# Optimization experiments

Hardware: AMD Instinct MI355X
Metric: run time of the kernel (lower is better)

Reference implementation:

```python
import jax, jax.numpy as jnp
import numpy as np

B, S, E = 4, 2048, 1024
H, D = 16, 64  # num_heads, attention_head_dim


def setup_inputs() -> dict:
    key = jax.random.key(0)
    ks = jax.random.split(key, 9)
    scale_e = 1.0 / np.sqrt(E)
    scale_hd = 1.0 / np.sqrt(H * D)
    x = jax.random.normal(ks[0], (B, S, E), dtype=jnp.float32)
    # per-head projection weights, stacked: [H, E, D]
    Wq = jax.random.uniform(ks[1], (H, E, D), minval=-scale_e, maxval=scale_e, dtype=jnp.float32)
    Wk = jax.random.uniform(ks[2], (H, E, D), minval=-scale_e, maxval=scale_e, dtype=jnp.float32)
    Wv = jax.random.uniform(ks[3], (H, E, D), minval=-scale_e, maxval=scale_e, dtype=jnp.float32)
    bq = jax.random.uniform(ks[4], (H, D), minval=-scale_e, maxval=scale_e, dtype=jnp.float32)
    bk = jax.random.uniform(ks[5], (H, D), minval=-scale_e, maxval=scale_e, dtype=jnp.float32)
    bv = jax.random.uniform(ks[6], (H, D), minval=-scale_e, maxval=scale_e, dtype=jnp.float32)
    Wo = jax.random.uniform(ks[7], (H * D, E), minval=-scale_hd, maxval=scale_hd, dtype=jnp.float32)
    bo = jax.random.uniform(ks[8], (E,), minval=-scale_hd, maxval=scale_hd, dtype=jnp.float32)
    return {"x": x, "Wq": Wq, "Wk": Wk, "Wv": Wv, "bq": bq, "bk": bk, "bv": bv, "Wo": Wo, "bo": bo}


def reference(x, Wq, Wk, Wv, bq, bk, bv, Wo, bo):
    # Per-head QKV projections, vectorized over heads: [B,H,S,D]
    Q = jnp.einsum('bse,hed->bhsd', x, Wq) + bq[None, :, None, :]
    K = jnp.einsum('bse,hed->bhsd', x, Wk) + bk[None, :, None, :]
    V = jnp.einsum('bse,hed->bhsd', x, Wv) + bv[None, :, None, :]
    scale = 1.0 / jnp.sqrt(jnp.asarray(D, dtype=Q.dtype))
    scores = jnp.einsum('bhsd,bhtd->bhst', Q, K) * scale  # [B,H,S,S]
    attn = jax.nn.softmax(scores, axis=-1)
    Z = jnp.einsum('bhst,bhtd->bhsd', attn, V)            # [B,H,S,D]
    # concat heads on feature dim -> [B,S,H*D], then output projection
    Zc = jnp.transpose(Z, (0, 2, 1, 3)).reshape(B, S, H * D)
    return Zc @ Wo + bo
```

## Files before the change

kernel.cpp:

```cpp
#include <hip/hip_runtime.h>


typedef __attribute__((ext_vector_type(4)))  float   f32x4;
typedef __attribute__((ext_vector_type(16))) float   f32x16;
typedef __attribute__((ext_vector_type(8)))  __bf16  bf16x8;
typedef __attribute__((ext_vector_type(4)))  __bf16  bf16x4;
typedef __attribute__((ext_vector_type(4)))  unsigned int u32x4;
typedef unsigned int u32;

#if __has_builtin(__builtin_amdgcn_exp2f)
#define EXP2F(x) __builtin_amdgcn_exp2f(x)
#else
#define EXP2F(x) exp2f(x)
#endif

__device__ __forceinline__ f32x4 fzero4() {
    f32x4 z = {0.f, 0.f, 0.f, 0.f};
    return z;
}
__device__ __forceinline__ f32x16 fzero16() {
    f32x16 z;
#pragma unroll
    for (int i = 0; i < 16; i++) z[i] = 0.f;
    return z;
}

__device__ __forceinline__ u32 cvtpk_bf16(float lo, float hi_) {
    u32 r;
    asm("v_cvt_pk_bf16_f32 %0, %1, %2" : "=v"(r) : "v"(lo), "v"(hi_));
    return r;
}

__device__ __forceinline__ void gload_lds16(const void* g, void* l) {
    __builtin_amdgcn_global_load_lds(
        (const __attribute__((address_space(1))) u32*)g,
        (__attribute__((address_space(3))) u32*)l, 16, 0, 0);
}

__global__ __launch_bounds__(256) void cvt_f32_bf16_4(
    const float* __restrict__ s, __bf16* __restrict__ d, long n) {
    long i = ((long)blockIdx.x * 256 + threadIdx.x) * 4;
    if (i >= n) return;
    float4 v = *(const float4*)(s + i);
    bf16x4 o = { (__bf16)v.x, (__bf16)v.y, (__bf16)v.z, (__bf16)v.w };
    *(bf16x4*)(d + i) = o;
}

__global__ __launch_bounds__(256) void pack_w_t(
    const float* __restrict__ src, __bf16* __restrict__ dst, int R, int C) {
    __shared__ float t[32][33];
    const int z = blockIdx.z;
    src += (size_t)z * R * C;
    dst += (size_t)z * R * C;
    const int r0 = blockIdx.x * 32, c0 = blockIdx.y * 32;
    const int x = threadIdx.x, y = threadIdx.y;
#pragma unroll
    for (int i = 0; i < 4; i++)
        t[y + i * 8][x] = src[(size_t)(r0 + y + i * 8) * C + c0 + x];
    __syncthreads();
#pragma unroll
    for (int i = 0; i < 4; i++)
        dst[(size_t)(c0 + y + i * 8) * R + r0 + x] = (__bf16)t[x][y + i * 8];
}

__global__ __launch_bounds__(256) void pack_bias(
    const float* __restrict__ bq, const float* __restrict__ bk,
    const float* __restrict__ bv, float* __restrict__ bqkv) {
    int n = blockIdx.x * 256 + threadIdx.x;
    if (n >= 3072) return;
    int t = n >> 10, r = n & 1023;
    const float* s = (t == 0) ? bq : (t == 1) ? bk : bv;
    bqkv[n] = s[r];
}

template <bool F32OUT>
__global__ __launch_bounds__(256) void gemm_bt(
    const __bf16* __restrict__ A, const __bf16* __restrict__ Bt,
    const float* __restrict__ bias, void* __restrict__ Cout,
    int M, int N, int K, int ldc) {
    __shared__ __bf16 As[128 * 32];
    __shared__ __bf16 Bs[128 * 32];
    const int tid  = threadIdx.x;
    const int lane = tid & 63, wid = tid >> 6;
    const int wr = wid >> 1, wc = wid & 1;
    const int l15 = lane & 15, l4 = lane >> 4;
    const int bn = blockIdx.x, bm = blockIdx.y;
    const long arow = (long)bm * 128 + (tid >> 2);
    const long brow = (long)bn * 128 + (tid >> 2);
    const int  kcol = (tid & 3) * 8;

    f32x4 acc[4][4];
#pragma unroll
    for (int i = 0; i < 4; i++)
#pragma unroll
        for (int j = 0; j < 4; j++) acc[i][j] = fzero4();

    for (int k0 = 0; k0 < K; k0 += 32) {
        gload_lds16(A + arow * K + k0 + kcol,        (char*)As + wid * 1024);
        gload_lds16(A + (arow + 64) * K + k0 + kcol, (char*)As + 4096 + wid * 1024);
        gload_lds16(Bt + brow * K + k0 + kcol,        (char*)Bs + wid * 1024);
        gload_lds16(Bt + (brow + 64) * K + k0 + kcol, (char*)Bs + 4096 + wid * 1024);
        __syncthreads();
        bf16x8 a[4], b[4];
#pragma unroll
        for (int mi = 0; mi < 4; mi++)
            a[mi] = *(const bf16x8*)&As[(wr * 64 + mi * 16 + l15) * 32 + l4 * 8];
#pragma unroll
        for (int ni = 0; ni < 4; ni++)
            b[ni] = *(const bf16x8*)&Bs[(wc * 64 + ni * 16 + l15) * 32 + l4 * 8];
#pragma unroll
        for (int mi = 0; mi < 4; mi++)
#pragma unroll
            for (int ni = 0; ni < 4; ni++)
                acc[mi][ni] = __builtin_amdgcn_mfma_f32_16x16x32_bf16(
                    a[mi], b[ni], acc[mi][ni], 0, 0, 0);
        __syncthreads();
    }

#pragma unroll
    for (int mi = 0; mi < 4; mi++)
#pragma unroll
        for (int ni = 0; ni < 4; ni++) {
            const int row = bm * 128 + wr * 64 + mi * 16 + l4 * 4;
            const int col = bn * 128 + wc * 64 + ni * 16 + l15;
            const float bv = bias ? bias[col] : 0.f;
#pragma unroll
            for (int r = 0; r < 4; r++) {
                float v = acc[mi][ni][r] + bv;
                if (F32OUT)
                    ((float*)Cout)[(long)(row + r) * ldc + col] = v;
                else
                    ((__bf16*)Cout)[(long)(row + r) * ldc + col] = (__bf16)v;
            }
        }
}

__global__ __launch_bounds__(256) void repack_vt(
    const __bf16* __restrict__ QKV, __bf16* __restrict__ VT) {
    __shared__ __bf16 t[32][33];
    const int s0 = blockIdx.x * 32, d0 = blockIdx.y * 32, bh = blockIdx.z;
    const int b = bh >> 4, h = bh & 15;
    const int x = threadIdx.x, y = threadIdx.y;
    const __bf16* src = QKV + (size_t)(b * 2048) * 3072 + 2048 + h * 64;
#pragma unroll
    for (int i = 0; i < 4; i++)
        t[y + i * 8][x] = src[(size_t)(s0 + y + i * 8) * 3072 + d0 + x];
    __syncthreads();
    __bf16* dst = VT + (size_t)bh * 64 * 2048;
#pragma unroll
    for (int i = 0; i < 4; i++)
        dst[(size_t)(d0 + y + i * 8) * 2048 + s0 + x] = t[x][y + i * 8];
}

__global__ __launch_bounds__(256, 4) void attn_fwd(
    const __bf16* __restrict__ QKV, const __bf16* __restrict__ VT,
    __bf16* __restrict__ Z) {
    const int S = 2048, LDQ = 3072;
    const int dd = blockIdx.x;
    const int blk = (dd & 7) * 128 + (dd >> 3);
    const int qt = blk & 15, bh = blk >> 4, b = bh >> 4, h = bh & 15;
    const int tid = threadIdx.x, wid = tid >> 6, lane = tid & 63;
    const int l31 = lane & 31, hi = lane >> 5;

    __shared__ __bf16 smem[16384];

    const __bf16* Qb = QKV + (size_t)b * S * LDQ + h * 64;
    const __bf16* Kb = Qb + 1024;
    const __bf16* Vb = VT + (size_t)bh * 64 * S;
    const int qrow = qt * 128 + wid * 32;

    bf16x8 qf[4];
#pragma unroll
    for (int kk = 0; kk < 4; kk++)
        qf[kk] = *(const bf16x8*)(Qb + (size_t)(qrow + l31) * LDQ + kk * 16 + hi * 8);

    const int f0 = wid * 2, f1 = wid * 2 + 1;
    const int kr0 = (f0 >> 2) * 32 + l31, kc0 = (f0 & 3) * 16 + hi * 8;
    const int kr1 = (f1 >> 2) * 32 + l31, kc1 = (f1 & 3) * 16 + hi * 8;
    const int vr0 = kr0, vs0 = kc0;
    const int vr1 = kr1, vs1 = kc1;
    const int ldst = lane * 16;

    f32x16 o0 = fzero16(), o1 = fzero16();
    float m_r = -1e30f, l_r = 0.f;
    const float csc = 0.18033688011f;

    gload_lds16(Kb + (size_t)kr0 * LDQ + kc0, (char*)smem + f0 * 1024 + ldst);
    gload_lds16(Kb + (size_t)kr1 * LDQ + kc1, (char*)smem + f1 * 1024 + ldst);
    gload_lds16(Vb + (size_t)vr0 * S + vs0,   (char*)smem + 16384 + f0 * 1024 + ldst);
    gload_lds16(Vb + (size_t)vr1 * S + vs1,   (char*)smem + 16384 + f1 * 1024 + ldst);
    asm volatile("s_waitcnt vmcnt(0)" ::: "memory");
    __syncthreads();

    int cur = 0;
    for (int t0 = 0; t0 < S; t0 += 64, cur ^= 1) {
        if (t0 + 64 < S) {
            char* kl = (char*)smem + (cur ^ 1) * 8192;
            char* vl = (char*)smem + 16384 + (cur ^ 1) * 8192;
            gload_lds16(Kb + (size_t)(t0 + 64 + kr0) * LDQ + kc0, kl + f0 * 1024 + ldst);
            gload_lds16(Kb + (size_t)(t0 + 64 + kr1) * LDQ + kc1, kl + f1 * 1024 + ldst);
            gload_lds16(Vb + (size_t)vr0 * S + t0 + 64 + vs0,     vl + f0 * 1024 + ldst);
            gload_lds16(Vb + (size_t)vr1 * S + t0 + 64 + vs1,     vl + f1 * 1024 + ldst);
        }
        const char* kbase = (const char*)smem + cur * 8192;
        const char* vbase = (const char*)smem + 16384 + cur * 8192;

        bf16x8 kf[8];
#pragma unroll
        for (int f = 0; f < 8; f++)
            kf[f] = *(const bf16x8*)(kbase + f * 1024 + ldst);
        f32x16 s0 = fzero16(), s1 = fzero16();
        __builtin_amdgcn_s_setprio(1);
#pragma unroll
        for (int kk = 0; kk < 4; kk++) {
            s0 = __builtin_amdgcn_mfma_f32_32x32x16_bf16(kf[kk],     qf[kk], s0, 0, 0, 0);
            s1 = __builtin_amdgcn_mfma_f32_32x32x16_bf16(kf[4 + kk], qf[kk], s1, 0, 0, 0);
        }
        __builtin_amdgcn_s_setprio(0);

        float mm[16];
#pragma unroll
        for (int i = 0; i < 16; i++) mm[i] = fmaxf(s0[i], s1[i]);
#pragma unroll
        for (int st = 8; st >= 1; st >>= 1)
#pragma unroll
            for (int i = 0; i < st; i++) mm[i] = fmaxf(mm[i], mm[i + st]);
        const float pm = fmaxf(mm[0], __shfl_xor(mm[0], 32));
        const float mnew = fmaxf(m_r, pm);
        const float alpha = EXP2F((m_r - mnew) * csc);
        m_r = mnew;
        l_r *= alpha;
#pragma unroll
        for (int i = 0; i < 16; i++) { o0[i] *= alpha; o1[i] *= alpha; }
        const float mc = m_r * csc;
        float ss[16];
#pragma unroll
        for (int i = 0; i < 16; i++) {
            float p0 = EXP2F(s0[i] * csc - mc); s0[i] = p0;
            float p1 = EXP2F(s1[i] * csc - mc); s1[i] = p1;
            ss[i] = p0 + p1;
        }
#pragma unroll
        for (int st = 8; st >= 1; st >>= 1)
#pragma unroll
            for (int i = 0; i < st; i++) ss[i] += ss[i + st];
        l_r += ss[0] + __shfl_xor(ss[0], 32);

#pragma unroll
        for (int kkt = 0; kkt < 4; kkt++) {
            const int r0 = (kkt & 1) * 8;
            u32 w0, w1, w2, w3;
            if (kkt < 2) {
                w0 = cvtpk_bf16(s0[r0],     s0[r0 + 1]);
                w1 = cvtpk_bf16(s0[r0 + 2], s0[r0 + 3]);
                w2 = cvtpk_bf16(s0[r0 + 4], s0[r0 + 5]);
                w3 = cvtpk_bf16(s0[r0 + 6], s0[r0 + 7]);
            } else {
                w0 = cvtpk_bf16(s1[r0],     s1[r0 + 1]);
                w1 = cvtpk_bf16(s1[r0 + 2], s1[r0 + 3]);
                w2 = cvtpk_bf16(s1[r0 + 4], s1[r0 + 5]);
                w3 = cvtpk_bf16(s1[r0 + 6], s1[r0 + 7]);
            }
            asm("v_permlane32_swap_b32 %0, %1" : "+v"(w0), "+v"(w2));
            asm("v_permlane32_swap_b32 %0, %1" : "+v"(w1), "+v"(w3));
            u32x4 pw = {w0, w1, w2, w3};
            bf16x8 pf = __builtin_bit_cast(bf16x8, pw);
            bf16x8 vf0 = *(const bf16x8*)(vbase + kkt * 1024 + ldst);
            bf16x8 vf1 = *(const bf16x8*)(vbase + (4 + kkt) * 1024 + ldst);
            __builtin_amdgcn_s_setprio(1);
            o0 = __builtin_amdgcn_mfma_f32_32x32x16_bf16(vf0, pf, o0, 0, 0, 0);
            o1 = __builtin_amdgcn_mfma_f32_32x32x16_bf16(vf1, pf, o1, 0, 0, 0);
            __builtin_amdgcn_s_setprio(0);
        }

        asm volatile("s_waitcnt vmcnt(0)" ::: "memory");
        __syncthreads();
    }

    const float inv = 1.0f / l_r;
    __bf16 (*Tl)[72] = (__bf16 (*)[72])smem;
    const int trow = wid * 32 + l31;
#pragma unroll
    for (int g = 0; g < 4; g++) {
        bf16x4 t4a, t4b;
#pragma unroll
        for (int j = 0; j < 4; j++) {
            t4a[j] = (__bf16)(o0[4 * g + j] * inv);
            t4b[j] = (__bf16)(o1[4 * g + j] * inv);
        }
        *(bf16x4*)&Tl[trow][g * 8 + hi * 4]      = t4a;
        *(bf16x4*)&Tl[trow][32 + g * 8 + hi * 4] = t4b;
    }
    asm volatile("s_waitcnt lgkmcnt(0)" ::: "memory");
    __builtin_amdgcn_sched_barrier(0);

    const int rr = wid * 32 + (lane >> 1);
    const int ch = (lane & 1) * 32;
#pragma unroll
    for (int i = 0; i < 4; i++) {
        bf16x8 z = *(const bf16x8*)&Tl[rr][ch + i * 8];
        *(bf16x8*)&Z[((size_t)b * S + qt * 128 + rr) * 1024 + h * 64 + ch + i * 8] = z;
    }
}

extern "C" void kernel_launch(void* const* d_in, const int* in_sizes, int n_in,
                              void* d_out, int out_size, void* d_ws, size_t ws_size,
                              hipStream_t stream) {
    const float* x  = (const float*)d_in[0];
    const float* Wq = (const float*)d_in[1];
    const float* Wk = (const float*)d_in[2];
    const float* Wv = (const float*)d_in[3];
    const float* bq = (const float*)d_in[4];
    const float* bk = (const float*)d_in[5];
    const float* bv = (const float*)d_in[6];
    const float* Wo = (const float*)d_in[7];
    const float* bo = (const float*)d_in[8];
    float* out = (float*)d_out;

    char* p = (char*)d_ws;
    __bf16* xb   = (__bf16*)p; p += 8192L * 1024 * 2;
    __bf16* Wqkv = (__bf16*)p; p += 3072L * 1024 * 2;
    float*  bqkv = (float*)p;  p += 3072L * 4;
    __bf16* QKV  = (__bf16*)p; p += 8192L * 3072 * 2;
    __bf16* VTb  = (__bf16*)p; p += 64L * 64 * 2048 * 2;
    __bf16* Zb   = (__bf16*)p; p += 8192L * 1024 * 2;
    __bf16* Wot  = (__bf16*)p; p += 1024L * 1024 * 2;

    cvt_f32_bf16_4<<<8192, 256, 0, stream>>>(x, xb, 8192L * 1024);
    pack_w_t<<<dim3(32, 2, 16), dim3(32, 8), 0, stream>>>(Wq, Wqkv,                1024, 64);
    pack_w_t<<<dim3(32, 2, 16), dim3(32, 8), 0, stream>>>(Wk, Wqkv + 1024L * 1024, 1024, 64);
    pack_w_t<<<dim3(32, 2, 16), dim3(32, 8), 0, stream>>>(Wv, Wqkv + 2048L * 1024, 1024, 64);
    pack_w_t<<<dim3(32, 32, 1), dim3(32, 8), 0, stream>>>(Wo, Wot, 1024, 1024);
    pack_bias<<<12, 256, 0, stream>>>(bq, bk, bv, bqkv);

    gemm_bt<false><<<dim3(24, 64), 256, 0, stream>>>(xb, Wqkv, bqkv, QKV,
                                                     8192, 3072, 1024, 3072);
    repack_vt<<<dim3(64, 2, 64), dim3(32, 8), 0, stream>>>(QKV, VTb);
    attn_fwd<<<1024, 256, 0, stream>>>(QKV, VTb, Zb);
    gemm_bt<true><<<dim3(8, 64), 256, 0, stream>>>(Zb, Wot, bo, out,
                                                   8192, 1024, 1024, 1024);
}
```

Measured before the change: 234.3 us.

## Fuse V transpose into QKV GEMM epilogue and skip unneeded softmax rescales

A dedicated QKV GEMM now writes the V slice straight into the transposed VT layout from its epilogue, so the separate repack_vt kernel launch and its extra read/write of V go away. The attention loop only rescales the running max and accumulators when some lane's new max exceeds the old one by more than a threshold (lazy rescaling). This avoids the exp and 32 multiplies per tile in the common case, but relies on the stale max keeping exp2 bounded. The priority raise is also hoisted to cover the whole PV MFMA loop instead of toggling per iteration.

```diff
diff --git a/kernel.cpp b/kernel.cpp
--- a/kernel.cpp
+++ b/kernel.cpp
@@ -135,21 +135,80 @@
         }
 }
 
-__global__ __launch_bounds__(256) void repack_vt(
-    const __bf16* __restrict__ QKV, __bf16* __restrict__ VT) {
-    __shared__ __bf16 t[32][33];
-    const int s0 = blockIdx.x * 32, d0 = blockIdx.y * 32, bh = blockIdx.z;
-    const int b = bh >> 4, h = bh & 15;
-    const int x = threadIdx.x, y = threadIdx.y;
-    const __bf16* src = QKV + (size_t)(b * 2048) * 3072 + 2048 + h * 64;
+__global__ __launch_bounds__(256) void gemm_qkv(
+    const __bf16* __restrict__ A, const __bf16* __restrict__ Bt,
+    const float* __restrict__ bias, __bf16* __restrict__ QKV,
+    __bf16* __restrict__ VT, int K) {
+    __shared__ __bf16 As[128 * 32];
+    __shared__ __bf16 Bs[128 * 32];
+    const int tid  = threadIdx.x;
+    const int lane = tid & 63, wid = tid >> 6;
+    const int wr = wid >> 1, wc = wid & 1;
+    const int l15 = lane & 15, l4 = lane >> 4;
+    const int bn = blockIdx.x, bm = blockIdx.y;
+    const long arow = (long)bm * 128 + (tid >> 2);
+    const long brow = (long)bn * 128 + (tid >> 2);
+    const int  kcol = (tid & 3) * 8;
+
+    f32x4 acc[4][4];
 #pragma unroll
     for (int i = 0; i < 4; i++)
-        t[y + i * 8][x] = src[(size_t)(s0 + y + i * 8) * 3072 + d0 + x];
-    __syncthreads();
-    __bf16* dst = VT + (size_t)bh * 64 * 2048;
-#pragma unroll
-    for (int i = 0; i < 4; i++)
-        dst[(size_t)(d0 + y + i * 8) * 2048 + s0 + x] = t[x][y + i * 8];
+#pragma unroll
+        for (int j = 0; j < 4; j++) acc[i][j] = fzero4();
+
+    for (int k0 = 0; k0 < K; k0 += 32) {
+        gload_lds16(A + arow * K + k0 + kcol,        (char*)As + wid * 1024);
+        gload_lds16(A + (arow + 64) * K + k0 + kcol, (char*)As + 4096 + wid * 1024);
+        gload_lds16(Bt + brow * K + k0 + kcol,        (char*)Bs + wid * 1024);
+        gload_lds16(Bt + (brow + 64) * K + k0 + kcol, (char*)Bs + 4096 + wid * 1024);
+        __syncthreads();
+        bf16x8 a[4], b[4];
+#pragma unroll
+        for (int mi = 0; mi < 4; mi++)
+            a[mi] = *(const bf16x8*)&As[(wr * 64 + mi * 16 + l15) * 32 + l4 * 8];
+#pragma unroll
+        for (int ni = 0; ni < 4; ni++)
+            b[ni] = *(const bf16x8*)&Bs[(wc * 64 + ni * 16 + l15) * 32 + l4 * 8];
+#pragma unroll
+        for (int mi = 0; mi < 4; mi++)
+#pragma unroll
+            for (int ni = 0; ni < 4; ni++)
+                acc[mi][ni] = __builtin_amdgcn_mfma_f32_16x16x32_bf16(
+                    a[mi], b[ni], acc[mi][ni], 0, 0, 0);
+        __syncthreads();
+    }
+
+    if (bn < 16) {
+#pragma unroll
+        for (int mi = 0; mi < 4; mi++)
+#pragma unroll
+            for (int ni = 0; ni < 4; ni++) {
+                const int row = bm * 128 + wr * 64 + mi * 16 + l4 * 4;
+                const int col = bn * 128 + wc * 64 + ni * 16 + l15;
+                const float bv = bias[col];
+#pragma unroll
+                for (int r = 0; r < 4; r++)
+                    QKV[(long)(row + r) * 3072 + col] =
+                        (__bf16)(acc[mi][ni][r] + bv);
+            }
+    } else {
+#pragma unroll
+        for (int mi = 0; mi < 4; mi++)
+#pragma unroll
+            for (int ni = 0; ni < 4; ni++) {
+                const int row = bm * 128 + wr * 64 + mi * 16 + l4 * 4;
+                const int col = bn * 128 + wc * 64 + ni * 16 + l15;
+                const float bv = bias[col];
+                const int vcol = col - 2048;
+                const int h = vcol >> 6, dcol = vcol & 63;
+                const int bb = row >> 11, s = row & 2047;
+                bf16x4 o;
+#pragma unroll
+                for (int r = 0; r < 4; r++)
+                    o[r] = (__bf16)(acc[mi][ni][r] + bv);
+                *(bf16x4*)&VT[((size_t)(bb * 16 + h) * 64 + dcol) * 2048 + s] = o;
+            }
+    }
 }
 
 __global__ __launch_bounds__(256, 4) void attn_fwd(
@@ -226,12 +285,14 @@
 #pragma unroll
             for (int i = 0; i < st; i++) mm[i] = fmaxf(mm[i], mm[i + st]);
         const float pm = fmaxf(mm[0], __shfl_xor(mm[0], 32));
-        const float mnew = fmaxf(m_r, pm);
-        const float alpha = EXP2F((m_r - mnew) * csc);
-        m_r = mnew;
-        l_r *= alpha;
-#pragma unroll
-        for (int i = 0; i < 16; i++) { o0[i] *= alpha; o1[i] *= alpha; }
+        if (!__all(pm - m_r <= 64.f)) {
+            const float mnew = fmaxf(m_r, pm);
+            const float alpha = EXP2F((m_r - mnew) * csc);
+            m_r = mnew;
+            l_r *= alpha;
+#pragma unroll
+            for (int i = 0; i < 16; i++) { o0[i] *= alpha; o1[i] *= alpha; }
+        }
         const float mc = m_r * csc;
         float ss[16];
 #pragma unroll
@@ -246,6 +307,7 @@
             for (int i = 0; i < st; i++) ss[i] += ss[i + st];
         l_r += ss[0] + __shfl_xor(ss[0], 32);
 
+        __builtin_amdgcn_s_setprio(1);
 #pragma unroll
         for (int kkt = 0; kkt < 4; kkt++) {
             const int r0 = (kkt & 1) * 8;
@@ -267,11 +329,10 @@
             bf16x8 pf = __builtin_bit_cast(bf16x8, pw);
             bf16x8 vf0 = *(const bf16x8*)(vbase + kkt * 1024 + ldst);
             bf16x8 vf1 = *(const bf16x8*)(vbase + (4 + kkt) * 1024 + ldst);
-            __builtin_amdgcn_s_setprio(1);
             o0 = __builtin_amdgcn_mfma_f32_32x32x16_bf16(vf0, pf, o0, 0, 0, 0);
             o1 = __builtin_amdgcn_mfma_f32_32x32x16_bf16(vf1, pf, o1, 0, 0, 0);
-            __builtin_amdgcn_s_setprio(0);
-        }
+        }
+        __builtin_amdgcn_s_setprio(0);
 
         asm volatile("s_waitcnt vmcnt(0)" ::: "memory");
         __syncthreads();
@@ -333,9 +394,7 @@
     pack_w_t<<<dim3(32, 32, 1), dim3(32, 8), 0, stream>>>(Wo, Wot, 1024, 1024);
     pack_bias<<<12, 256, 0, stream>>>(bq, bk, bv, bqkv);
 
-    gemm_bt<false><<<dim3(24, 64), 256, 0, stream>>>(xb, Wqkv, bqkv, QKV,
-                                                     8192, 3072, 1024, 3072);
-    repack_vt<<<dim3(64, 2, 64), dim3(32, 8), 0, stream>>>(QKV, VTb);
+    gemm_qkv<<<dim3(24, 64), 256, 0, stream>>>(xb, Wqkv, bqkv, QKV, VTb, 1024);
     attn_fwd<<<1024, 256, 0, stream>>>(QKV, VTb, Zb);
     gemm_bt<true><<<dim3(8, 64), 256, 0, stream>>>(Zb, Wot, bo, out,
                                                    8192, 1024, 1024, 1024);
```

Measured after the change: 234.2 us. No clear change (-0.0%).
